# Kernel optimization log

Hardware: AMD Instinct MI355X
Metric: run time of the kernel (lower is better)

The kernel has to match this reference:

```python
import jax, jax.numpy as jnp
import numpy as np

B, T, F, H, L = 256, 512, 64, 256, 2
DH = 2 * H          # decoder hidden size (bidirectional encoder concat)
OUT, OSL = 2, 20    # output_size, output_seq_len


def gru_cell(x, h, Wih, Whh, bih, bhh):
    # PyTorch GRU cell, gate order (r, z, n)
    gi = x @ Wih.T + bih
    gh = h @ Whh.T + bhh
    ir, iz, inn = jnp.split(gi, 3, axis=-1)
    hr, hz, hn = jnp.split(gh, 3, axis=-1)
    r = jax.nn.sigmoid(ir + hr)
    z = jax.nn.sigmoid(iz + hz)
    n = jnp.tanh(inn + r * hn)
    return (1.0 - z) * n + z * h


def setup_inputs() -> dict:
    key = jax.random.key(0)
    ks = iter(jax.random.split(key, 32))
    def p(shape, scale=0.05):
        return jax.random.normal(next(ks), shape, dtype=jnp.float32) * scale
    inp = {
        "x": p((B, T, F), 1.0),
        "start_token": jnp.zeros((1, 1, OUT), jnp.float32),
        # encoder layer 0 (input F), layer 1 (input 2H); axis 0 = direction (fwd, bwd)
        "enc_Wih0": p((2, 3 * H, F)), "enc_Whh0": p((2, 3 * H, H)),
        "enc_bih0": p((2, 3 * H)),   "enc_bhh0": p((2, 3 * H)),
        "enc_Wih1": p((2, 3 * H, 2 * H)), "enc_Whh1": p((2, 3 * H, H)),
        "enc_bih1": p((2, 3 * H)),   "enc_bhh1": p((2, 3 * H)),
        # decoder: unidirectional, hidden DH; layer0 input OUT, layer1 input DH
        "dec_Wih0": p((3 * DH, OUT)), "dec_Whh0": p((3 * DH, DH)),
        "dec_bih0": p((3 * DH,)),    "dec_bhh0": p((3 * DH,)),
        "dec_Wih1": p((3 * DH, DH)), "dec_Whh1": p((3 * DH, DH)),
        "dec_bih1": p((3 * DH,)),    "dec_bhh1": p((3 * DH,)),
        "fc_W": p((OUT, DH)), "fc_b": p((OUT,)),
    }
    return inp


def _run_dir(xs, Wih, Whh, bih, bhh, reverse):
    # xs: [T, B, Fin] -> (ys [T, B, H], h_T [B, H])
    h0 = jnp.zeros((xs.shape[1], Whh.shape[1]), xs.dtype)
    def step(h, xt):
        hn = gru_cell(xt, h, Wih, Whh, bih, bhh)
        return hn, hn
    hT, ys = jax.lax.scan(step, h0, xs, reverse=reverse)
    return ys, hT


def reference(x, start_token,
              enc_Wih0, enc_Whh0, enc_bih0, enc_bhh0,
              enc_Wih1, enc_Whh1, enc_bih1, enc_bhh1,
              dec_Wih0, dec_Whh0, dec_bih0, dec_bhh0,
              dec_Wih1, dec_Whh1, dec_bih1, dec_bhh1,
              fc_W, fc_b):
    b = x.shape[0]
    xs = jnp.swapaxes(x, 0, 1)  # [T, B, F]
    enc_layers = [(enc_Wih0, enc_Whh0, enc_bih0, enc_bhh0),
                  (enc_Wih1, enc_Whh1, enc_bih1, enc_bhh1)]
    hiddens = []
    layer_in = xs
    for (Wih, Whh, bih, bhh) in enc_layers:
        yf, hf = _run_dir(layer_in, Wih[0], Whh[0], bih[0], bhh[0], reverse=False)
        yb, hb = _run_dir(layer_in, Wih[1], Whh[1], bih[1], bhh[1], reverse=True)
        layer_in = jnp.concatenate([yf, yb], axis=-1)   # [T, B, 2H]
        hiddens.append(jnp.concatenate([hf, hb], axis=-1))  # [B, 2H] = cat(fwd, bwd)
    inp0 = jnp.broadcast_to(start_token, (b, 1, OUT))[:, 0]  # [B, OUT]
    def dec_step(carry, _):
        inp, (h0, h1) = carry
        h0n = gru_cell(inp, h0, dec_Wih0, dec_Whh0, dec_bih0, dec_bhh0)
        h1n = gru_cell(h0n, h1, dec_Wih1, dec_Whh1, dec_bih1, dec_bhh1)
        pred = h1n @ fc_W.T + fc_b
        return (pred, (h0n, h1n)), pred
    _, preds = jax.lax.scan(dec_step, (inp0, (hiddens[0], hiddens[1])), None, length=OSL)
    return jnp.swapaxes(preds, 0, 1)  # [B, OSL, OUT]
```

## Files before the change

### kernel.cpp

```cpp
#include <hip/hip_runtime.h>
#include <hip/hip_bf16.h>
#include <stdint.h>
#include <stddef.h>


typedef __bf16 bf16_t;
typedef bf16_t bf16x8 __attribute__((ext_vector_type(8)));
typedef float  f32x4  __attribute__((ext_vector_type(4)));

#define B_   256
#define T_   512
#define F_   64
#define H_   256
#define G_   768
#define DH_  512
#define DG_  1536
#define OSL_ 20

__device__ __forceinline__ float sigm(float x) {
    float e = __builtin_amdgcn_exp2f(-1.442695040888963f * x);
    return __builtin_amdgcn_rcpf(1.0f + e);
}
__device__ __forceinline__ float tanh_(float x) {
    float e = __builtin_amdgcn_exp2f(-2.885390081777927f * x);
    return __builtin_amdgcn_rcpf(1.0f + e) * 2.0f - 1.0f;
}

__device__ __forceinline__ bf16x8 load_f32x8_as_bf16(const float* p) {
    f32x4 u = *(const f32x4*)p;
    f32x4 v = *(const f32x4*)(p + 4);
    bf16x8 r;
    r[0]=(bf16_t)u[0]; r[1]=(bf16_t)u[1]; r[2]=(bf16_t)u[2]; r[3]=(bf16_t)u[3];
    r[4]=(bf16_t)v[0]; r[5]=(bf16_t)v[1]; r[6]=(bf16_t)v[2]; r[7]=(bf16_t)v[3];
    return r;
}

__global__ __launch_bounds__(256) void prep_all(
    const float* __restrict__ s0, const float* __restrict__ s1,
    const float* __restrict__ s2, const float* __restrict__ s3,
    const float* __restrict__ s4, const float* __restrict__ s5,
    const float* __restrict__ s6,
    bf16_t* __restrict__ d0, bf16_t* __restrict__ d1, bf16_t* __restrict__ d2,
    bf16_t* __restrict__ d3, bf16_t* __restrict__ d4, bf16_t* __restrict__ d5,
    bf16_t* __restrict__ d6,
    const float* __restrict__ wih0d, const float* __restrict__ fcw,
    const float* __restrict__ fcb, const float* __restrict__ bih0d,
    const float* __restrict__ st, bf16_t* __restrict__ weff,
    float* __restrict__ beff, float* __restrict__ ov,
    unsigned int* __restrict__ bar) {
    int i = blockIdx.x * 256 + threadIdx.x;
    switch (blockIdx.y) {
      case 0: if (i < 2*G_*F_)  d0[i] = (bf16_t)s0[i]; break;
      case 1: if (i < 2*G_*H_)  d1[i] = (bf16_t)s1[i]; break;
      case 2: if (i < 2*G_*DH_) d2[i] = (bf16_t)s2[i]; break;
      case 3: if (i < 2*G_*H_)  d3[i] = (bf16_t)s3[i]; break;
      case 4: if (i < DG_*DH_)  d4[i] = (bf16_t)s4[i]; break;
      case 5: if (i < DG_*DH_)  d5[i] = (bf16_t)s5[i]; break;
      case 6: if (i < DG_*DH_)  d6[i] = (bf16_t)s6[i]; break;
      default: {
        if (i < 1024) bar[i] = 0u;
        if (i < DG_*DH_) {
          int g = i >> 9, k = i & 511;
          float a0 = wih0d[g * 2], a1 = wih0d[g * 2 + 1];
          weff[i] = (bf16_t)(a0 * fcw[k] + a1 * fcw[DH_ + k]);
          if (k == 0) {
            beff[g] = a0 * fcb[0] + a1 * fcb[1] + bih0d[g];
            ov[g]   = a0 * st[0]  + a1 * st[1]  + bih0d[g];
          }
        }
      } break;
    }
}

__global__ __launch_bounds__(256) void gemm_gi(
    const float* __restrict__ x, const bf16_t* __restrict__ xcat,
    const bf16_t* __restrict__ Bt, bf16_t* __restrict__ gi, int t0, int K) {
    __shared__ bf16_t As[128 * 64];
    __shared__ bf16_t Bs[128 * 64];
    int m0 = blockIdx.x * 128, n0 = blockIdx.y * 128;
    int tid = threadIdx.x;
    int lane = tid & 63, w = tid >> 6;
    int col = lane & 15, quad = lane >> 4;
    int qm = (w >> 1) * 64, qn = (w & 1) * 64;

    int tl = m0 >> 8;
    int bbase = m0 & 255;
    int t_real = t0 + tl;
    if (n0 >= 768) t_real = (T_ - 1) - t_real;

    f32x4 acc[4][4] = {};
    for (int k0 = 0; k0 < K; k0 += 64) {
        __syncthreads();
#pragma unroll
        for (int i = 0; i < 4; i++) {
            int c = i * 256 + tid;
            int m = c >> 3, kc = c & 7;
            int kcs = kc ^ (m & 7);
            bf16x8 av;
            if (K == 64) {
                av = load_f32x8_as_bf16(x + ((size_t)(bbase + m) * T_ + t_real) * F_ + kcs * 8);
            } else {
                av = *(const bf16x8*)(xcat + ((size_t)t_real * B_ + bbase + m) * DH_ + k0 + kcs * 8);
            }
            *(bf16x8*)(&As[c * 8]) = av;
            *(bf16x8*)(&Bs[c * 8]) = *(const bf16x8*)(Bt + (size_t)(n0 + m) * K + k0 + kcs * 8);
        }
        __syncthreads();
#pragma unroll
        for (int kt = 0; kt < 2; kt++) {
            bf16x8 a[4], b[4];
#pragma unroll
            for (int mt = 0; mt < 4; mt++) {
                int r = qm + mt * 16 + col;
                a[mt] = *(const bf16x8*)(&As[(r * 8 + ((kt * 4 + quad) ^ (r & 7))) * 8]);
                int rn = qn + mt * 16 + col;
                b[mt] = *(const bf16x8*)(&Bs[(rn * 8 + ((kt * 4 + quad) ^ (rn & 7))) * 8]);
            }
#pragma unroll
            for (int mt = 0; mt < 4; mt++)
#pragma unroll
                for (int nt = 0; nt < 4; nt++)
                    acc[mt][nt] = __builtin_amdgcn_mfma_f32_16x16x32_bf16(a[mt], b[nt], acc[mt][nt], 0, 0, 0);
        }
    }
#pragma unroll
    for (int mt = 0; mt < 4; mt++)
#pragma unroll
        for (int nt = 0; nt < 4; nt++)
#pragma unroll
            for (int i = 0; i < 4; i++) {
                int row = m0 + qm + mt * 16 + quad * 4 + i;
                int cg  = n0 + qn + nt * 16 + col;
                gi[(size_t)row * DG_ + cg] = (bf16_t)acc[mt][nt][i];
            }
}

__global__ __launch_bounds__(512) void gru_scan(
    const bf16_t* __restrict__ gi, int t0, int tc,
    const bf16_t* __restrict__ whh,
    const float* __restrict__ bih, const float* __restrict__ bhh,
    float* __restrict__ hstate, bf16_t* __restrict__ y, float* __restrict__ hT) {
    __shared__ bf16_t gi_lds[16 * 768];
    __shared__ bf16_t h_lds[2 * 16 * 264];

    int dir = blockIdx.x >> 4;
    int b0  = (blockIdx.x & 15) * 16;
    int tid = threadIdx.x;
    int w = tid >> 6, lane = tid & 63, col = lane & 15, quad = lane >> 4;

    bf16x8 wf[3][2][8];
    const bf16_t* wbase = whh + (size_t)dir * G_ * H_;
#pragma unroll
    for (int g = 0; g < 3; g++)
#pragma unroll
        for (int nt = 0; nt < 2; nt++) {
            int row = g * 256 + w * 32 + nt * 16 + col;
#pragma unroll
            for (int kt = 0; kt < 8; kt++)
                wf[g][nt][kt] = *(const bf16x8*)(wbase + (size_t)row * H_ + kt * 32 + quad * 8);
        }
    float brz[2][2], bin_[2], bhn[2];
#pragma unroll
    for (int nt = 0; nt < 2; nt++) {
        int j = w * 32 + nt * 16 + col;
        brz[0][nt] = bih[dir * G_ + j] + bhh[dir * G_ + j];
        brz[1][nt] = bih[dir * G_ + 256 + j] + bhh[dir * G_ + 256 + j];
        bin_[nt]   = bih[dir * G_ + 512 + j];
        bhn[nt]    = bhh[dir * G_ + 512 + j];
    }
    int bb[3], oo[3];
#pragma unroll
    for (int it = 0; it < 3; it++) {
        int c = it * 512 + tid;
        bb[it] = c / 96;
        oo[it] = (c % 96) * 8;
    }
    float hold[2][4];
#pragma unroll
    for (int nt = 0; nt < 2; nt++)
#pragma unroll
        for (int i = 0; i < 4; i++) {
            int j = w * 32 + nt * 16 + col;
            hold[nt][i] = t0 ? hstate[dir * 65536 + (b0 + quad * 4 + i) * 256 + j] : 0.0f;
        }
    for (int i = tid; i < 16 * 264; i += 512) {
        int b = i / 264, j = i % 264;
        float v = (t0 && j < 256) ? hstate[dir * 65536 + (b0 + b) * 256 + j] : 0.0f;
        h_lds[i] = (bf16_t)v;
    }
#pragma unroll
    for (int it = 0; it < 3; it++) {
        int c = it * 512 + tid;
        *(bf16x8*)(&gi_lds[c * 8]) =
            *(const bf16x8*)(gi + ((size_t)0 * B_ + b0 + bb[it]) * DG_ + dir * G_ + oo[it]);
    }
    __syncthreads();

    for (int s = 0; s < tc; s++) {
        int par = s & 1;
        int t = t0 + s;
        int sn = (s + 1 < tc) ? (s + 1) : s;

        bf16x8 pg[3];
#pragma unroll
        for (int it = 0; it < 3; it++)
            pg[it] = *(const bf16x8*)(gi + ((size_t)sn * B_ + b0 + bb[it]) * DG_ + dir * G_ + oo[it]);

        f32x4 acc[3][2] = {};
        const bf16_t* hcur = &h_lds[par * 4224];
#pragma unroll
        for (int kt = 0; kt < 8; kt++) {
            bf16x8 af = *(const bf16x8*)(hcur + col * 264 + kt * 32 + quad * 8);
#pragma unroll
            for (int g = 0; g < 3; g++)
#pragma unroll
                for (int nt = 0; nt < 2; nt++)
                    acc[g][nt] = __builtin_amdgcn_mfma_f32_16x16x32_bf16(af, wf[g][nt][kt], acc[g][nt], 0, 0, 0);
        }

        bf16_t* hnext = &h_lds[(par ^ 1) * 4224];
        int tp = dir ? (T_ - 1 - t) : t;
#pragma unroll
        for (int nt = 0; nt < 2; nt++) {
            int j = w * 32 + nt * 16 + col;
#pragma unroll
            for (int i = 0; i < 4; i++) {
                int b = quad * 4 + i;
                float gr = acc[0][nt][i] + (float)gi_lds[b * 768 + j]       + brz[0][nt];
                float gz = acc[1][nt][i] + (float)gi_lds[b * 768 + 256 + j] + brz[1][nt];
                float gn = (float)gi_lds[b * 768 + 512 + j] + bin_[nt];
                float r = sigm(gr), z = sigm(gz);
                float n = tanh_(gn + r * (acc[2][nt][i] + bhn[nt]));
                float hv = (1.0f - z) * n + z * hold[nt][i];
                hold[nt][i] = hv;
                hnext[b * 264 + j] = (bf16_t)hv;
                if (y) y[((size_t)tp * B_ + b0 + b) * DH_ + dir * H_ + j] = (bf16_t)hv;
                if (t == T_ - 1) hT[(size_t)(b0 + b) * DH_ + dir * H_ + j] = hv;
            }
        }
        __syncthreads();
#pragma unroll
        for (int it = 0; it < 3; it++)
            *(bf16x8*)(&gi_lds[(it * 512 + tid) * 8]) = pg[it];
        __syncthreads();
    }
#pragma unroll
    for (int nt = 0; nt < 2; nt++)
#pragma unroll
        for (int i = 0; i < 4; i++) {
            int j = w * 32 + nt * 16 + col;
            hstate[dir * 65536 + (b0 + quad * 4 + i) * 256 + j] = hold[nt][i];
        }
}


__device__ __forceinline__ void gbar(unsigned int* cnt) {
    __syncthreads();
    if (threadIdx.x == 0) {
        __hip_atomic_fetch_add(cnt, 1u, __ATOMIC_RELEASE, __HIP_MEMORY_SCOPE_AGENT);
        unsigned int s = 0;
        while (__hip_atomic_load(cnt, __ATOMIC_RELAXED, __HIP_MEMORY_SCOPE_AGENT) < 8u
               && ++s < (1u << 20))
            __builtin_amdgcn_s_sleep(2);
    }
    __syncthreads();
}

__device__ __forceinline__ void stage16(bf16_t* lds, const bf16_t* src) {
    const char* s = (const char*)src;
    char* d = (char*)lds;
#pragma unroll
    for (int i2 = 0; i2 < 8; ++i2) {
        int off = i2 * 2048 + threadIdx.x * 8;
        unsigned long long v = __hip_atomic_load(
            (const unsigned long long*)(s + off),
            __ATOMIC_RELAXED, __HIP_MEMORY_SCOPE_AGENT);
        int row = off >> 10;
        int swz = off ^ ((row & 7) << 4);
        *(unsigned long long*)(d + swz) = v;
    }
}

__device__ __forceinline__ bf16x8 fragrd(const bf16_t* lds, int kt, int col, int quad) {
    int byte = (col * 1024 + kt * 64 + quad * 16) ^ ((col & 7) << 4);
    return *(const bf16x8*)((const char*)lds + byte);
}

__device__ __forceinline__ void publish(bf16_t* dst, int b, int j, float hv, int col) {
    bf16_t hb = (bf16_t)hv;
    unsigned short mb;
    __builtin_memcpy(&mb, &hb, 2);
    unsigned int pv = (unsigned int)__shfl_xor((int)(unsigned int)mb, 1);
    if ((col & 1) == 0) {
        unsigned int word = (unsigned int)mb | (pv << 16);
        __hip_atomic_store((unsigned int*)((char*)dst + (size_t)(b * DH_ + j) * 2),
                           word, __ATOMIC_RELAXED, __HIP_MEMORY_SCOPE_AGENT);
    }
}

__device__ __forceinline__ void cell_step(
    const bf16_t* sh, const bf16_t* sx, bool dox,
    const bf16_t* __restrict__ Wx, const bf16_t* __restrict__ Wh,
    int j, int col, int quad, int grp,
    float br, float bz, float bin_, float bhn,
    float hold[4], bf16_t* hout, float* hist_t) {
    f32x4 aR = {}, aZ = {}, aIN = {}, aHN = {};
#pragma unroll
    for (int kt = 0; kt < 16; ++kt) {
        bf16x8 ah = fragrd(sh, kt, col, quad);
        bf16x8 w0 = *(const bf16x8*)(Wh + (size_t)j * DH_ + kt * 32 + quad * 8);
        bf16x8 w1 = *(const bf16x8*)(Wh + (size_t)(DH_ + j) * DH_ + kt * 32 + quad * 8);
        bf16x8 w2 = *(const bf16x8*)(Wh + (size_t)(2 * DH_ + j) * DH_ + kt * 32 + quad * 8);
        aR  = __builtin_amdgcn_mfma_f32_16x16x32_bf16(ah, w0, aR, 0, 0, 0);
        aZ  = __builtin_amdgcn_mfma_f32_16x16x32_bf16(ah, w1, aZ, 0, 0, 0);
        aHN = __builtin_amdgcn_mfma_f32_16x16x32_bf16(ah, w2, aHN, 0, 0, 0);
        if (dox) {
            bf16x8 ax = fragrd(sx, kt, col, quad);
            bf16x8 x0 = *(const bf16x8*)(Wx + (size_t)j * DH_ + kt * 32 + quad * 8);
            bf16x8 x1 = *(const bf16x8*)(Wx + (size_t)(DH_ + j) * DH_ + kt * 32 + quad * 8);
            bf16x8 x2 = *(const bf16x8*)(Wx + (size_t)(2 * DH_ + j) * DH_ + kt * 32 + quad * 8);
            aR  = __builtin_amdgcn_mfma_f32_16x16x32_bf16(ax, x0, aR, 0, 0, 0);
            aZ  = __builtin_amdgcn_mfma_f32_16x16x32_bf16(ax, x1, aZ, 0, 0, 0);
            aIN = __builtin_amdgcn_mfma_f32_16x16x32_bf16(ax, x2, aIN, 0, 0, 0);
        }
    }
#pragma unroll
    for (int i = 0; i < 4; ++i) {
        int b = grp * 16 + quad * 4 + i;
        float r = sigm(aR[i] + br);
        float z = sigm(aZ[i] + bz);
        float n = tanh_(aIN[i] + bin_ + r * (aHN[i] + bhn));
        float hv = (1.0f - z) * n + z * hold[i];
        hold[i] = hv;
        if (hist_t) hist_t[(size_t)b * DH_ + j] = hv;
        publish(hout, b, j, hv, col);
    }
}

__global__ __launch_bounds__(256) void dec_persist(
    const bf16_t* __restrict__ weff, const float* __restrict__ beff,
    const float* __restrict__ ov,
    const bf16_t* __restrict__ wdhh0, const float* __restrict__ dbhh0,
    const bf16_t* __restrict__ wdih1, const float* __restrict__ dbih1,
    const bf16_t* __restrict__ wdhh1, const float* __restrict__ dbhh1,
    const float* __restrict__ h0init, const float* __restrict__ h1init,
    bf16_t* hx00, bf16_t* hx01, bf16_t* hx10, bf16_t* hx11,
    float* __restrict__ hist, unsigned int* __restrict__ bar) {
    __shared__ bf16_t sh[16 * 512];
    __shared__ bf16_t sx[16 * 512];
    int grp = blockIdx.x & 15;
    int jblk = blockIdx.x >> 4;
    int tid = threadIdx.x, w = tid >> 6, lane = tid & 63;
    int col = lane & 15, quad = lane >> 4;
    int j = jblk * 64 + w * 16 + col;

    float b0r = beff[j] + dbhh0[j],           b0z = beff[DH_ + j] + dbhh0[DH_ + j];
    float b0in = beff[2 * DH_ + j],           b0hn = dbhh0[2 * DH_ + j];
    float o0r = ov[j] + dbhh0[j],             o0z = ov[DH_ + j] + dbhh0[DH_ + j];
    float o0in = ov[2 * DH_ + j];
    float b1r = dbih1[j] + dbhh1[j],          b1z = dbih1[DH_ + j] + dbhh1[DH_ + j];
    float b1in = dbih1[2 * DH_ + j],          b1hn = dbhh1[2 * DH_ + j];

    float hold0[4], hold1[4];
#pragma unroll
    for (int i = 0; i < 4; ++i) {
        int b = grp * 16 + quad * 4 + i;
        float v0 = h0init[(size_t)b * DH_ + j];
        float v1 = h1init[(size_t)b * DH_ + j];
        hold0[i] = v0; hold1[i] = v1;
        publish(hx01, b, j, v0, col);
        publish(hx11, b, j, v1, col);
    }
    gbar(bar + grp);

    int ph = 1;
    for (int t = 0; t < OSL_; ++t) {
        bf16_t* write0 = (t & 1) ? hx01 : hx00;
        bf16_t* read0  = (t & 1) ? hx00 : hx01;
        bf16_t* write1 = (t & 1) ? hx11 : hx10;
        bf16_t* read1  = (t & 1) ? hx10 : hx11;

        bool dox0 = (t > 0);
        __syncthreads();
        stage16(sh, read0 + (size_t)grp * 16 * DH_);
        if (dox0) stage16(sx, read1 + (size_t)grp * 16 * DH_);
        __syncthreads();
        cell_step(sh, sx, dox0, weff, wdhh0, j, col, quad, grp,
                  dox0 ? b0r : o0r, dox0 ? b0z : o0z, dox0 ? b0in : o0in, b0hn,
                  hold0, write0, nullptr);
        gbar(bar + ph * 16 + grp); ph++;

        __syncthreads();
        stage16(sh, read1 + (size_t)grp * 16 * DH_);
        stage16(sx, write0 + (size_t)grp * 16 * DH_);
        __syncthreads();
        cell_step(sh, sx, true, wdih1, wdhh1, j, col, quad, grp,
                  b1r, b1z, b1in, b1hn,
                  hold1, write1, hist + (size_t)t * B_ * DH_);
        gbar(bar + ph * 16 + grp); ph++;
    }
}

__global__ __launch_bounds__(256) void fc_all(
    const float* __restrict__ hist, const float* __restrict__ fcw,
    const float* __restrict__ fcb, float* __restrict__ out) {
    int t  = blockIdx.x >> 4;
    int b0 = (blockIdx.x & 15) * 16;
    int tid = threadIdx.x;
    int bl = tid >> 4, o = (tid >> 3) & 1, part = tid & 7;
    const float* hp = hist + ((size_t)t * B_ + b0 + bl) * DH_;
    const float* wp = fcw + o * DH_;
    float s = 0.0f;
    for (int k = part * 64; k < part * 64 + 64; k += 4) {
        f32x4 hv = *(const f32x4*)(hp + k);
        f32x4 wv = *(const f32x4*)(wp + k);
        s += hv[0] * wv[0] + hv[1] * wv[1] + hv[2] * wv[2] + hv[3] * wv[3];
    }
    s += __shfl_down(s, 4); s += __shfl_down(s, 2); s += __shfl_down(s, 1);
    if (part == 0) out[(size_t)(b0 + bl) * (OSL_ * 2) + t * 2 + o] = s + fcb[o];
}


#define OFF_WIH0E 0ull
#define OFF_WHH0E 196608ull
#define OFF_WIH1E 983040ull
#define OFF_WHH1E 2555904ull
#define OFF_WDHH0 3342336ull
#define OFF_WDIH1 4915200ull
#define OFF_WDHH1 6488064ull
#define OFF_WEFF  8060928ull
#define OFF_BEFF  9633792ull
#define OFF_BAR   9641984ull
#define OFF_OV    9658368ull
#define OFF_H0A   9682944ull
#define OFF_H0B   10207232ull
#define OFF_H1A   10731520ull
#define OFF_H1B   11255808ull
#define OFF_HST   11780096ull
#define OFF_HIST  12304384ull
#define OFF_XCAT  22790144ull
#define OFF_GI    157007872ull

extern "C" void kernel_launch(void* const* d_in, const int* in_sizes, int n_in,
                              void* d_out, int out_size, void* d_ws, size_t ws_size,
                              hipStream_t stream) {
    const float* x      = (const float*)d_in[0];
    const float* st     = (const float*)d_in[1];
    const float* eWih0  = (const float*)d_in[2];
    const float* eWhh0  = (const float*)d_in[3];
    const float* ebih0  = (const float*)d_in[4];
    const float* ebhh0  = (const float*)d_in[5];
    const float* eWih1  = (const float*)d_in[6];
    const float* eWhh1  = (const float*)d_in[7];
    const float* ebih1  = (const float*)d_in[8];
    const float* ebhh1  = (const float*)d_in[9];
    const float* dWih0  = (const float*)d_in[10];
    const float* dWhh0  = (const float*)d_in[11];
    const float* dbih0  = (const float*)d_in[12];
    const float* dbhh0  = (const float*)d_in[13];
    const float* dWih1  = (const float*)d_in[14];
    const float* dWhh1  = (const float*)d_in[15];
    const float* dbih1  = (const float*)d_in[16];
    const float* dbhh1  = (const float*)d_in[17];
    const float* fcW    = (const float*)d_in[18];
    const float* fcb    = (const float*)d_in[19];

    char* ws = (char*)d_ws;
    bf16_t* wih0e = (bf16_t*)(ws + OFF_WIH0E);
    bf16_t* whh0e = (bf16_t*)(ws + OFF_WHH0E);
    bf16_t* wih1e = (bf16_t*)(ws + OFF_WIH1E);
    bf16_t* whh1e = (bf16_t*)(ws + OFF_WHH1E);
    bf16_t* wdhh0 = (bf16_t*)(ws + OFF_WDHH0);
    bf16_t* wdih1 = (bf16_t*)(ws + OFF_WDIH1);
    bf16_t* wdhh1 = (bf16_t*)(ws + OFF_WDHH1);
    bf16_t* weff  = (bf16_t*)(ws + OFF_WEFF);
    float*  beff  = (float*)(ws + OFF_BEFF);
    unsigned int* bar = (unsigned int*)(ws + OFF_BAR);
    float*  ovp   = (float*)(ws + OFF_OV);
    float*  h0init = (float*)(ws + OFF_H0A);
    float*  h1init = (float*)(ws + OFF_H1A);
    bf16_t* hx00  = (bf16_t*)(ws + OFF_H0B);
    bf16_t* hx01  = (bf16_t*)(ws + OFF_H0B + 262144ull);
    bf16_t* hx10  = (bf16_t*)(ws + OFF_H1B);
    bf16_t* hx11  = (bf16_t*)(ws + OFF_H1B + 262144ull);
    float*  hstate = (float*)(ws + OFF_HST);
    float*  hist  = (float*)(ws + OFF_HIST);
    bf16_t* xcat  = (bf16_t*)(ws + OFF_XCAT);
    bf16_t* gi    = (bf16_t*)(ws + OFF_GI);

    int Tc = 512;
    while (Tc > 8 && OFF_GI + (unsigned long long)Tc * 786432ull > (unsigned long long)ws_size)
        Tc >>= 1;
    int nch = T_ / Tc;

    prep_all<<<dim3(3072, 8), 256, 0, stream>>>(
        eWih0, eWhh0, eWih1, eWhh1, dWhh0, dWih1, dWhh1,
        wih0e, whh0e, wih1e, whh1e, wdhh0, wdih1, wdhh1,
        dWih0, fcW, fcb, dbih0, st, weff, beff, ovp, bar);

    for (int c = 0; c < nch; c++) {
        gemm_gi<<<dim3(Tc * 2, 12), 256, 0, stream>>>(x, nullptr, wih0e, gi, c * Tc, 64);
        gru_scan<<<32, 512, 0, stream>>>(gi, c * Tc, Tc, whh0e, ebih0, ebhh0, hstate, xcat, h0init);
    }
    for (int c = 0; c < nch; c++) {
        gemm_gi<<<dim3(Tc * 2, 12), 256, 0, stream>>>(nullptr, xcat, wih1e, gi, c * Tc, 512);
        gru_scan<<<32, 512, 0, stream>>>(gi, c * Tc, Tc, whh1e, ebih1, ebhh1, hstate, nullptr, h1init);
    }

    dec_persist<<<128, 256, 0, stream>>>(weff, beff, ovp,
                                         wdhh0, dbhh0, wdih1, dbih1, wdhh1, dbhh1,
                                         h0init, h1init,
                                         hx00, hx01, hx10, hx11,
                                         hist, bar);

    fc_all<<<OSL_ * 16, 256, 0, stream>>>(hist, fcW, fcb, (float*)d_out);
}
```

Before: 4.798 ms.

## Reuse LDS-staged decoder states across layers and use L2-coherent wide loads

Inside the decoder loop, the layer-0 output staged for layer 1 is kept in LDS and reused as the next step's layer-0 hidden input. This removes one staging pass and one __syncthreads per half-step, and the last grid barrier is skipped. Staging now uses inline-asm 16-byte global loads with the sc0 cache bit in place of 8-byte atomic loads, and the publish store becomes a plain store instead of an atomic. The barrier spin sleep is also shortened. The plain stores and asm loads depend on cache-coherence behaviour across workgroups, which carries a risk of reading stale data.

```diff
diff --git a/kernel.cpp b/kernel.cpp
--- a/kernel.cpp
+++ b/kernel.cpp
@@ -261,23 +261,31 @@
         unsigned int s = 0;
         while (__hip_atomic_load(cnt, __ATOMIC_RELAXED, __HIP_MEMORY_SCOPE_AGENT) < 8u
                && ++s < (1u << 20))
-            __builtin_amdgcn_s_sleep(2);
+            __builtin_amdgcn_s_sleep(1);
     }
     __syncthreads();
 }
 
-__device__ __forceinline__ void stage16(bf16_t* lds, const bf16_t* src) {
+__device__ __forceinline__ void stage16_l2(bf16_t* lds, const bf16_t* src) {
+    f32x4 v0, v1, v2, v3;
     const char* s = (const char*)src;
-    char* d = (char*)lds;
-#pragma unroll
-    for (int i2 = 0; i2 < 8; ++i2) {
-        int off = i2 * 2048 + threadIdx.x * 8;
-        unsigned long long v = __hip_atomic_load(
-            (const unsigned long long*)(s + off),
-            __ATOMIC_RELAXED, __HIP_MEMORY_SCOPE_AGENT);
+    const char* a0 = s + threadIdx.x * 16;
+    asm volatile(
+        "global_load_dwordx4 %0, %4, off sc0\n\t"
+        "global_load_dwordx4 %1, %5, off sc0\n\t"
+        "global_load_dwordx4 %2, %6, off sc0\n\t"
+        "global_load_dwordx4 %3, %7, off sc0\n\t"
+        "s_waitcnt vmcnt(0)"
+        : "=&v"(v0), "=&v"(v1), "=&v"(v2), "=&v"(v3)
+        : "v"(a0), "v"(a0 + 4096), "v"(a0 + 8192), "v"(a0 + 12288)
+        : "memory");
+    f32x4 vv[4] = { v0, v1, v2, v3 };
+#pragma unroll
+    for (int i2 = 0; i2 < 4; ++i2) {
+        int off = i2 * 4096 + threadIdx.x * 16;
         int row = off >> 10;
         int swz = off ^ ((row & 7) << 4);
-        *(unsigned long long*)(d + swz) = v;
+        *(f32x4*)((char*)lds + swz) = vv[i2];
     }
 }
 
@@ -293,8 +301,7 @@
     unsigned int pv = (unsigned int)__shfl_xor((int)(unsigned int)mb, 1);
     if ((col & 1) == 0) {
         unsigned int word = (unsigned int)mb | (pv << 16);
-        __hip_atomic_store((unsigned int*)((char*)dst + (size_t)(b * DH_ + j) * 2),
-                           word, __ATOMIC_RELAXED, __HIP_MEMORY_SCOPE_AGENT);
+        *(unsigned int*)((char*)dst + (size_t)(b * DH_ + j) * 2) = word;
     }
 }
 
@@ -379,25 +386,22 @@
         bf16_t* read0  = (t & 1) ? hx00 : hx01;
         bf16_t* write1 = (t & 1) ? hx11 : hx10;
         bf16_t* read1  = (t & 1) ? hx10 : hx11;
-
         bool dox0 = (t > 0);
-        __syncthreads();
-        stage16(sh, read0 + (size_t)grp * 16 * DH_);
-        if (dox0) stage16(sx, read1 + (size_t)grp * 16 * DH_);
+
+        if (t == 0) stage16_l2(sh, read0 + (size_t)grp * 16 * DH_);
+        stage16_l2(sx, read1 + (size_t)grp * 16 * DH_);
         __syncthreads();
         cell_step(sh, sx, dox0, weff, wdhh0, j, col, quad, grp,
                   dox0 ? b0r : o0r, dox0 ? b0z : o0z, dox0 ? b0in : o0in, b0hn,
                   hold0, write0, nullptr);
         gbar(bar + ph * 16 + grp); ph++;
 
+        stage16_l2(sh, write0 + (size_t)grp * 16 * DH_);
         __syncthreads();
-        stage16(sh, read1 + (size_t)grp * 16 * DH_);
-        stage16(sx, write0 + (size_t)grp * 16 * DH_);
-        __syncthreads();
-        cell_step(sh, sx, true, wdih1, wdhh1, j, col, quad, grp,
+        cell_step(sx, sh, true, wdih1, wdhh1, j, col, quad, grp,
                   b1r, b1z, b1in, b1hn,
                   hold1, write1, hist + (size_t)t * B_ * DH_);
-        gbar(bar + ph * 16 + grp); ph++;
+        if (t < OSL_ - 1) { gbar(bar + ph * 16 + grp); ph++; }
     }
 }
 
```

Result: no change. 4.770 ms (-0.6%).
